# Optimization experiments

Measured on AMD Instinct MI355X. Metric: run time of the kernel, lower is better.

Reference implementation:

```python
import jax, jax.numpy as jnp
import numpy as np

HEADS = 8
DIM = 512
DIM_HEAD = 64          # dim // 8
LANDMARKS = 256        # dim // 2
PINV_ITERS = 6
KERNEL = 33            # residual_conv_kernel
SCALE = DIM_HEAD ** -0.5
LN_EPS = 1e-5


def _moore_penrose_pinv(x, iters):
    # x: [B,H,m,m]; global (over all batches/heads) max of row/col abs sums, as in torch impl
    abs_x = jnp.abs(x)
    col = abs_x.sum(-1).max()
    row = abs_x.sum(-2).max()
    z = jnp.swapaxes(x, -1, -2) / (col * row)
    I = jnp.eye(x.shape[-1], dtype=x.dtype)
    for _ in range(iters):
        xz = x @ z
        z = 0.25 * z @ (13.0 * I - (xz @ (15.0 * I - (xz @ (7.0 * I - xz)))))
    return z


def setup_inputs() -> dict:
    key = jax.random.key(0)
    ks = jax.random.split(key, 5)
    B, N = 4, 8192
    x = jax.random.normal(ks[0], (B, N, DIM), dtype=jnp.float32)
    ln_g = jnp.ones((DIM,), jnp.float32)
    ln_b = jnp.zeros((DIM,), jnp.float32)
    w_qkv = jax.random.normal(ks[1], (DIM, 3 * HEADS * DIM_HEAD), jnp.float32) * 0.02
    w_out = jax.random.normal(ks[2], (HEADS * DIM_HEAD, DIM), jnp.float32) * 0.02
    b_out = jnp.zeros((DIM,), jnp.float32)
    res_kernel = jax.random.normal(ks[3], (HEADS, 1, KERNEL, 1), jnp.float32) * 0.02  # OIHW depthwise
    return {"x": x, "ln_g": ln_g, "ln_b": ln_b, "w_qkv": w_qkv,
            "w_out": w_out, "b_out": b_out, "res_kernel": res_kernel}


def reference(x, ln_g, ln_b, w_qkv, w_out, b_out, res_kernel):
    B, N, D = x.shape
    # pre-norm LayerNorm
    mu = x.mean(-1, keepdims=True)
    var = jnp.mean((x - mu) ** 2, axis=-1, keepdims=True)
    xn = (x - mu) * jax.lax.rsqrt(var + LN_EPS) * ln_g + ln_b
    # left-pad sequence so it divides into LANDMARKS groups (torch pads at front)
    m = LANDMARKS
    pad = (m - N % m) % m
    xp = jnp.pad(xn, ((0, 0), (pad, 0), (0, 0)))
    Np = N + pad
    qkv = xp @ w_qkv                                    # [B,Np,3*H*dh]
    q, k, v = jnp.split(qkv, 3, axis=-1)
    split_heads = lambda t: t.reshape(B, Np, HEADS, DIM_HEAD).transpose(0, 2, 1, 3)
    q, k, v = split_heads(q), split_heads(k), split_heads(v)  # [B,H,Np,dh]
    q = q * SCALE
    l = Np // m                                         # landmark group size
    q_l = q.reshape(B, HEADS, m, l, DIM_HEAD).sum(3) / l  # [B,H,m,dh]
    k_l = k.reshape(B, HEADS, m, l, DIM_HEAD).sum(3) / l
    sim1 = jnp.einsum('bhid,bhjd->bhij', q, k_l)        # [B,H,Np,m]
    sim2 = jnp.einsum('bhid,bhjd->bhij', q_l, k_l)      # [B,H,m,m]
    sim3 = jnp.einsum('bhid,bhjd->bhij', q_l, k)        # [B,H,m,Np]
    attn1 = jax.nn.softmax(sim1, axis=-1)
    attn2 = jax.nn.softmax(sim2, axis=-1)
    attn3 = jax.nn.softmax(sim3, axis=-1)
    attn2_inv = _moore_penrose_pinv(attn2, PINV_ITERS)
    out = (attn1 @ attn2_inv) @ (attn3 @ v)             # [B,H,Np,dh]
    # depthwise conv residual over sequence dim (Conv2d kernel (33,1), groups=heads)
    res = jax.lax.conv_general_dilated(
        v, res_kernel, window_strides=(1, 1),
        padding=[(KERNEL // 2, KERNEL // 2), (0, 0)],
        dimension_numbers=('NCHW', 'OIHW', 'NCHW'),
        feature_group_count=HEADS)
    out = out + res
    out = out.transpose(0, 2, 1, 3).reshape(B, Np, HEADS * DIM_HEAD)
    out = out @ w_out + b_out                           # dropout = identity (eval)
    out = out[:, -N:]                                   # drop front padding
    return x + out
```

## Files before the change

### kernel.cpp

```cpp
#include <hip/hip_runtime.h>
#include <hip/hip_bf16.h>
#include <stdint.h>

#define B_ 4
#define H_ 8
#define N_ 8192
#define D_ 512
#define M_ 256
#define BH 32
#define TOK 32768
#define SCALE 0.125f
#define LN_EPS 1e-5f

using bf16x8 = __attribute__((ext_vector_type(8))) short;
using f32x4  = __attribute__((ext_vector_type(4))) float;
typedef unsigned short u16;
typedef unsigned int   u32;

__device__ __forceinline__ float bf2f(u16 h){ union{u32 u; float f;} x; x.u = ((u32)h)<<16; return x.f; }
__device__ __forceinline__ u16 f2bf(float f){ union{float f; u32 u;} x; x.f=f; u32 r = (x.u + 0x7fffu + ((x.u>>16)&1u))>>16; return (u16)r; }
__device__ __forceinline__ f32x4 mfma16(bf16x8 a, bf16x8 b, f32x4 c){
  return __builtin_amdgcn_mfma_f32_16x16x32_bf16(a, b, c, 0, 0, 0);
}
__device__ __forceinline__ void stage16(const u16* g, u16* lds){
  __builtin_amdgcn_global_load_lds((const __attribute__((address_space(1))) unsigned int*)g,
                                   (__attribute__((address_space(3))) unsigned int*)lds, 16, 0, 0);
}

__global__ __launch_bounds__(256) void k_prep(const float* __restrict__ wqkv, const float* __restrict__ wout,
                                              u16* __restrict__ wqkvt, u16* __restrict__ woutt){
  int id = blockIdx.x*256 + threadIdx.x;
  for (int i = id; i < 1536*512; i += gridDim.x*256){ int c = i>>9, kk = i&511; wqkvt[i] = f2bf(wqkv[(size_t)kk*1536 + c]); }
  for (int i = id; i < 512*512;  i += gridDim.x*256){ int c = i>>9, kk = i&511; woutt[i] = f2bf(wout[(size_t)kk*512 + c]); }
}

__global__ __launch_bounds__(256) void k_ln(const float* __restrict__ x, const float* __restrict__ g,
                                            const float* __restrict__ bb, u16* __restrict__ xn){
  int row = blockIdx.x; int tid = threadIdx.x;
  const float* xr = x + (size_t)row*D_;
  float2 v = reinterpret_cast<const float2*>(xr)[tid];
  float s1 = v.x + v.y, s2 = v.x*v.x + v.y*v.y;
  for (int o=1;o<64;o<<=1){ s1 += __shfl_xor(s1,o); s2 += __shfl_xor(s2,o); }
  __shared__ float a1[4], a2[4];
  if ((tid&63)==0){ a1[tid>>6]=s1; a2[tid>>6]=s2; }
  __syncthreads();
  s1 = a1[0]+a1[1]+a1[2]+a1[3]; s2 = a2[0]+a2[1]+a2[2]+a2[3];
  float mu = s1*(1.f/D_);
  float var = s2*(1.f/D_) - mu*mu;
  float rs = rsqrtf(var + LN_EPS);
  float2 gg = reinterpret_cast<const float2*>(g)[tid];
  float2 b2 = reinterpret_cast<const float2*>(bb)[tid];
  u16 o0 = f2bf((v.x-mu)*rs*gg.x + b2.x);
  u16 o1 = f2bf((v.y-mu)*rs*gg.y + b2.y);
  reinterpret_cast<u32*>(xn + (size_t)row*D_)[tid] = (u32)o0 | ((u32)o1<<16);
}

__global__ __launch_bounds__(256) void k_qkv(const u16* __restrict__ A, const u16* __restrict__ Bt,
    u16* __restrict__ q, u16* __restrict__ k, u16* __restrict__ vt){
  __shared__ __align__(16) u16 As[2][128*32];
  __shared__ __align__(16) u16 Bs[2][128*32];
  int m0 = blockIdx.x*128, n0 = blockIdx.y*128;
  int tid = threadIdx.x, lane = tid&63, wave = tid>>6;
  int wm = wave>>1, wn = wave&1;
  int lr = lane>>2, lc = (lane&3)*8;
  f32x4 acc[4][4];
  #pragma unroll
  for (int i=0;i<4;i++)
    #pragma unroll
    for (int j=0;j<4;j++) acc[i][j] = (f32x4)0.f;

  auto stage_tile = [&](int k0, int buf){
    #pragma unroll
    for (int i=0;i<2;i++){
      int c = wave + i*4;
      stage16(&A [(size_t)(m0 + c*16 + lr)*512 + k0 + lc], &As[buf][c*16*32]);
      stage16(&Bt[(size_t)(n0 + c*16 + lr)*512 + k0 + lc], &Bs[buf][c*16*32]);
    }
  };
  stage_tile(0, 0);
  for (int it=0; it<16; it++){
    int cur = it&1;
    if (it<15){
      stage_tile((it+1)*32, cur^1);
      asm volatile("s_waitcnt vmcnt(4)" ::: "memory");
    } else {
      asm volatile("s_waitcnt vmcnt(0)" ::: "memory");
    }
    __syncthreads();
    bf16x8 a[4], b[4];
    #pragma unroll
    for (int mi=0;mi<4;mi++) a[mi] = *reinterpret_cast<const bf16x8*>(&As[cur][(wm*64+mi*16+(lane&15))*32 + (lane>>4)*8]);
    #pragma unroll
    for (int ni=0;ni<4;ni++) b[ni] = *reinterpret_cast<const bf16x8*>(&Bs[cur][(wn*64+ni*16+(lane&15))*32 + (lane>>4)*8]);
    #pragma unroll
    for (int mi=0;mi<4;mi++)
      #pragma unroll
      for (int ni=0;ni<4;ni++)
        acc[mi][ni] = mfma16(a[mi], b[ni], acc[mi][ni]);
    __syncthreads();
  }
  #pragma unroll
  for (int mi=0;mi<4;mi++){
    int gr0 = m0 + wm*64 + mi*16 + ((lane>>4)<<2);
    #pragma unroll
    for (int ni=0;ni<4;ni++){
      int gc = n0 + wn*64 + ni*16 + (lane&15);
      int t = gc>>9, wi = gc&511, h = wi>>6, d = wi&63;
      #pragma unroll
      for (int r=0;r<4;r++){
        int row = gr0 + r; int bq = row>>13, n = row & (N_-1);
        float val = acc[mi][ni][r];
        size_t bhh = (size_t)(bq*H_+h);
        if (t==0)      q[(bhh*N_ + n)*64 + d] = f2bf(val*SCALE);
        else if (t==1) k[(bhh*N_ + n)*64 + d] = f2bf(val);
        else           vt[(bhh*64 + d)*N_ + n] = f2bf(val);
      }
    }
  }
}

__global__ __launch_bounds__(64) void k_land(const u16* __restrict__ q, const u16* __restrict__ k,
                                             u16* __restrict__ ql, u16* __restrict__ kl){
  int bh = blockIdx.x >> 8, j = blockIdx.x & 255, d = threadIdx.x;
  size_t base = ((size_t)bh*N_ + j*32)*64 + d;
  float sq=0.f, sk=0.f;
  #pragma unroll
  for (int i=0;i<32;i++){ sq += bf2f(q[base + (size_t)i*64]); sk += bf2f(k[base + (size_t)i*64]); }
  size_t o = ((size_t)bh*256 + j)*64 + d;
  ql[o] = f2bf(sq*(1.f/32.f)); kl[o] = f2bf(sk*(1.f/32.f));
}

__global__ __launch_bounds__(256) void k_attn2(const u16* __restrict__ ql, const u16* __restrict__ kl,
                                               float* __restrict__ X, float* __restrict__ Xt){
  int bh = blockIdx.x >> 8, i = blockIdx.x & 255, j = threadIdx.x;
  __shared__ float qrow[64];
  __shared__ float red[256];
  if (j < 64) qrow[j] = bf2f(ql[((size_t)bh*256+i)*64 + j]);
  __syncthreads();
  const u16* kr = kl + ((size_t)bh*256 + j)*64;
  float s = 0.f;
  #pragma unroll
  for (int d=0; d<64; d++) s += qrow[d]*bf2f(kr[d]);
  red[j] = s; __syncthreads();
  for (int o=128;o>0;o>>=1){ if (j<o) red[j] = fmaxf(red[j], red[j+o]); __syncthreads(); }
  float mx = red[0]; __syncthreads();
  float e = __expf(s - mx);
  red[j] = e; __syncthreads();
  for (int o=128;o>0;o>>=1){ if (j<o) red[j] += red[j+o]; __syncthreads(); }
  float p = e / red[0];
  X [((size_t)bh*256+i)*256 + j] = p;
  Xt[((size_t)bh*256+j)*256 + i] = p;
}

__global__ __launch_bounds__(256) void k_pinvstats(const float* __restrict__ X, float* __restrict__ sc){
  int bh = blockIdx.x, t = threadIdx.x;
  const float* Xb = X + ((size_t)bh<<16);
  float cs=0.f, rs=0.f;
  for (int i=0;i<256;i++) cs += Xb[(size_t)i*256 + t];
  for (int j=0;j<256;j++) rs += Xb[(size_t)t*256 + j];
  __shared__ float r1[256], r2[256];
  r1[t]=cs; r2[t]=rs; __syncthreads();
  for (int o=128;o>0;o>>=1){ if (t<o){ r1[t]=fmaxf(r1[t],r1[t+o]); r2[t]=fmaxf(r2[t],r2[t+o]); } __syncthreads(); }
  if (t==0) sc[bh] = 1.f/(r1[0]*r2[0]);
}

__global__ __launch_bounds__(256) void k_pinvinit(const float* __restrict__ X, const float* __restrict__ Xt,
     const float* __restrict__ sc, u16* Xhi, u16* Xlo, u16* Znhi, u16* Znlo, u16* Zthi, u16* Ztlo){
  size_t i = (size_t)blockIdx.x*256 + threadIdx.x;
  int bh = (int)(i>>16);
  float s = sc[bh];
  float xv = X[i];  u16 h1 = f2bf(xv);  Xhi[i]=h1;  Xlo[i]=f2bf(xv - bf2f(h1));
  float zn = Xt[i]*s; u16 h2 = f2bf(zn); Znhi[i]=h2; Znlo[i]=f2bf(zn - bf2f(h2));
  float zt = xv*s;  u16 h3 = f2bf(zt);  Zthi[i]=h3; Ztlo[i]=f2bf(zt - bf2f(h3));
}

template<int MODE>
__global__ __launch_bounds__(256) void k_mmhl(
    const u16* Ahi, const u16* Alo,
    const u16* Bthi, const u16* Btlo,
    u16* Chi, u16* Clo,
    const u16* Znhi, const u16* Znlo,
    const u16* B1hi, const u16* B1lo,
    const u16* B2hi, const u16* B2lo,
    u16* Zothi, u16* Zotlo)
{
  __shared__ __align__(16) u16 AhS[2][64*32];
  __shared__ __align__(16) u16 AlS[2][64*32];
  __shared__ __align__(16) u16 BhS[2][64*32];
  __shared__ __align__(16) u16 BlS[2][64*32];
  int bh = blockIdx.z;
  int m0 = blockIdx.x*64, n0 = blockIdx.y*64;
  size_t base = ((size_t)bh)<<16;
  int tid = threadIdx.x, lane = tid&63, wave = tid>>6;
  int wm = wave>>1, wn = wave&1;
  int lr = lane>>2, lc = (lane&3)*8;
  f32x4 acc[2][2];
  #pragma unroll
  for (int i=0;i<2;i++)
    #pragma unroll
    for (int j=0;j<2;j++) acc[i][j] = (f32x4)0.f;

  auto stage_tile = [&](int k0, int buf){
    stage16(&Ahi [base + (size_t)(m0 + wave*16 + lr)*256 + k0 + lc], &AhS[buf][wave*16*32]);
    stage16(&Alo [base + (size_t)(m0 + wave*16 + lr)*256 + k0 + lc], &AlS[buf][wave*16*32]);
    stage16(&Bthi[base + (size_t)(n0 + wave*16 + lr)*256 + k0 + lc], &BhS[buf][wave*16*32]);
    stage16(&Btlo[base + (size_t)(n0 + wave*16 + lr)*256 + k0 + lc], &BlS[buf][wave*16*32]);
  };
  stage_tile(0, 0);
  for (int it=0; it<8; it++){
    int cur = it&1;
    if (it<7){
      stage_tile((it+1)*32, cur^1);
      asm volatile("s_waitcnt vmcnt(4)" ::: "memory");
    } else {
      asm volatile("s_waitcnt vmcnt(0)" ::: "memory");
    }
    __syncthreads();
    bf16x8 ah[2], al2[2], bh2[2], bl2[2];
    #pragma unroll
    for (int mi=0;mi<2;mi++){
      int rr = wm*32 + mi*16 + (lane&15);
      ah[mi]  = *reinterpret_cast<const bf16x8*>(&AhS[cur][rr*32 + (lane>>4)*8]);
      al2[mi] = *reinterpret_cast<const bf16x8*>(&AlS[cur][rr*32 + (lane>>4)*8]);
    }
    #pragma unroll
    for (int ni=0;ni<2;ni++){
      int rr = wn*32 + ni*16 + (lane&15);
      bh2[ni] = *reinterpret_cast<const bf16x8*>(&BhS[cur][rr*32 + (lane>>4)*8]);
      bl2[ni] = *reinterpret_cast<const bf16x8*>(&BlS[cur][rr*32 + (lane>>4)*8]);
    }
    #pragma unroll
    for (int mi=0;mi<2;mi++)
      #pragma unroll
      for (int ni=0;ni<2;ni++){
        f32x4 c = acc[mi][ni];
        c = mfma16(ah[mi],  bh2[ni], c);
        c = mfma16(ah[mi],  bl2[ni], c);
        c = mfma16(al2[mi], bh2[ni], c);
        acc[mi][ni] = c;
      }
    __syncthreads();
  }
  #pragma unroll
  for (int mi=0;mi<2;mi++){
    #pragma unroll
    for (int ni=0;ni<2;ni++){
      int gr0 = m0 + wm*32 + mi*16 + ((lane>>4)<<2);
      int gc  = n0 + wn*32 + ni*16 + (lane&15);
      #pragma unroll
      for (int rr=0;rr<4;rr++){
        int gr = gr0 + rr;
        float val = acc[mi][ni][rr];
        if (MODE==0){
          size_t o = base + (size_t)gr*256 + gc;
          u16 hh = f2bf(val); Chi[o]=hh; Clo[o]=f2bf(val - bf2f(hh));
        } else if (MODE==1){
          size_t o = base + (size_t)gc*256 + gr;
          u16 hh = f2bf(val); Chi[o]=hh; Clo[o]=f2bf(val - bf2f(hh));
        } else {
          size_t o = base + (size_t)gr*256 + gc;
          float z  = bf2f(Znhi[o]) + bf2f(Znlo[o]);
          float b1 = bf2f(B1hi[o]) + bf2f(B1lo[o]);
          float b2 = bf2f(B2hi[o]) + bf2f(B2lo[o]);
          float zn = 0.25f*(13.f*z - 15.f*b1 + 7.f*b2 - val);
          u16 hh = f2bf(zn); u16 ll = f2bf(zn - bf2f(hh));
          Chi[o] = hh; Clo[o] = ll;
          size_t ot = base + (size_t)gc*256 + gr;
          Zothi[ot] = hh; Zotlo[ot] = ll;
        }
      }
    }
  }
}

__global__ __launch_bounds__(256) void k_flashw(const u16* __restrict__ ql, const u16* __restrict__ kb,
                                                const u16* __restrict__ vt,
                                                float* __restrict__ part, float* __restrict__ lpart){
  __shared__ __align__(16) u16 P[4][64][40];
  int kc = blockIdx.x, bh = blockIdx.y;
  int tid = threadIdx.x, lane = tid&63, wave = tid>>6;
  bf16x8 aq[4][2];
  #pragma unroll
  for (int mi=0;mi<4;mi++){
    int row = wave*64 + mi*16 + (lane&15);
    #pragma unroll
    for (int ks=0;ks<2;ks++)
      aq[mi][ks] = *reinterpret_cast<const bf16x8*>(&ql[((size_t)bh*256 + row)*64 + ks*32 + (lane>>4)*8]);
  }
  f32x4 acc[4][4];
  float rs[4][4];
  #pragma unroll
  for (int i=0;i<4;i++)
    #pragma unroll
    for (int j=0;j<4;j++){ acc[i][j] = (f32x4)0.f; rs[i][j] = 0.f; }
  for (int step=0; step<16; step++){
    int nb = kc*512 + step*32;
    f32x4 s[4][2];
    #pragma unroll
    for (int ci=0;ci<2;ci++){
      int j = nb + ci*16 + (lane&15);
      const u16* kr = &kb[((size_t)bh*N_ + j)*64 + (lane>>4)*8];
      bf16x8 b0 = *reinterpret_cast<const bf16x8*>(kr);
      bf16x8 b1 = *reinterpret_cast<const bf16x8*>(kr + 32);
      #pragma unroll
      for (int mi=0;mi<4;mi++)
        s[mi][ci] = mfma16(aq[mi][1], b1, mfma16(aq[mi][0], b0, (f32x4)0.f));
    }
    #pragma unroll
    for (int mi=0;mi<4;mi++)
      #pragma unroll
      for (int ci=0;ci<2;ci++)
        #pragma unroll
        for (int rr=0;rr<4;rr++){
          float e = __expf(s[mi][ci][rr]);
          rs[mi][rr] += e;
          P[wave][mi*16 + ((lane>>4)<<2) + rr][ci*16 + (lane&15)] = f2bf(e);
        }
    __syncthreads();
    bf16x8 ap[4];
    #pragma unroll
    for (int mi=0;mi<4;mi++)
      ap[mi] = *reinterpret_cast<const bf16x8*>(&P[wave][mi*16 + (lane&15)][(lane>>4)*8]);
    #pragma unroll
    for (int ci=0;ci<4;ci++){
      int d = ci*16 + (lane&15);
      bf16x8 bv = *reinterpret_cast<const bf16x8*>(&vt[((size_t)bh*64 + d)*N_ + nb + (lane>>4)*8]);
      #pragma unroll
      for (int mi=0;mi<4;mi++)
        acc[mi][ci] = mfma16(ap[mi], bv, acc[mi][ci]);
    }
    __syncthreads();
  }
  #pragma unroll
  for (int mi=0;mi<4;mi++)
    #pragma unroll
    for (int rr=0;rr<4;rr++){
      float v2 = rs[mi][rr];
      v2 += __shfl_xor(v2,1); v2 += __shfl_xor(v2,2); v2 += __shfl_xor(v2,4); v2 += __shfl_xor(v2,8);
      rs[mi][rr] = v2;
    }
  size_t pb = ((size_t)kc*32 + bh)*256;
  #pragma unroll
  for (int mi=0;mi<4;mi++){
    int r0 = wave*64 + mi*16 + ((lane>>4)<<2);
    #pragma unroll
    for (int ci=0;ci<4;ci++){
      int d = ci*16 + (lane&15);
      #pragma unroll
      for (int rr=0;rr<4;rr++)
        part[(pb + r0 + rr)*64 + d] = acc[mi][ci][rr];
    }
    if ((lane&15)==0){
      #pragma unroll
      for (int rr=0;rr<4;rr++)
        lpart[pb + r0 + rr] = rs[mi][rr];
    }
  }
}

__global__ __launch_bounds__(256) void k_wfin(const float* __restrict__ part, const float* __restrict__ lpart,
                                              float* __restrict__ w){
  int idx = blockIdx.x*256 + threadIdx.x;
  int bh = idx>>14, within = idx & 16383, r = within>>6;
  float s = 0.f, l = 0.f;
  #pragma unroll
  for (int c=0;c<16;c++){
    s += part [(size_t)(c*32+bh)*16384 + within];
    l += lpart[(size_t)(c*32+bh)*256 + r];
  }
  w[idx] = s / l;
}

__global__ __launch_bounds__(64) void k_w2(const u16* __restrict__ Zhi, const u16* __restrict__ Zlo,
                                           const float* __restrict__ w, u16* __restrict__ w2t){
  int bh = blockIdx.x>>8, j = blockIdx.x&255, d = threadIdx.x;
  size_t zb = ((size_t)bh<<16) + (size_t)j*256;
  float acc = 0.f;
  for (int i=0;i<256;i++){
    float zv = bf2f(Zhi[zb+i]) + bf2f(Zlo[zb+i]);
    acc += zv * w[((size_t)bh*256 + i)*64 + d];
  }
  w2t[((size_t)bh*64 + d)*256 + j] = f2bf(acc);
}

__global__ __launch_bounds__(256) void k_conv(const u16* __restrict__ vt, const float* __restrict__ kern,
                                              u16* __restrict__ res_t){
  int t = threadIdx.x;
  int d = blockIdx.y, bh = blockIdx.z;
  int n0 = blockIdx.x*2048 + t*8;
  const u16* src = vt + ((size_t)bh*64 + d)*N_;
  const float* kh = kern + (bh&7)*33;
  float xv[40];
  #pragma unroll
  for (int vv=0; vv<5; vv++){
    int nb = n0 - 16 + vv*8;
    if (nb >= 0 && nb + 8 <= N_) {
      bf16x8 raw = *reinterpret_cast<const bf16x8*>(src + nb);
      #pragma unroll
      for (int j=0;j<8;j++) xv[vv*8+j] = bf2f((u16)raw[j]);
    } else {
      #pragma unroll
      for (int j=0;j<8;j++){
        int n = nb + j;
        xv[vv*8+j] = (n>=0 && n<N_) ? bf2f(src[n]) : 0.f;
      }
    }
  }
  float c[33];
  #pragma unroll
  for (int kk2=0;kk2<33;kk2++) c[kk2] = kh[kk2];
  u16 outv[8];
  #pragma unroll
  for (int j=0;j<8;j++){
    float acc = 0.f;
    #pragma unroll
    for (int kk2=0;kk2<33;kk2++) acc += xv[j+kk2]*c[kk2];
    outv[j] = f2bf(acc);
  }
  *reinterpret_cast<bf16x8*>(res_t + ((size_t)bh*64 + d)*N_ + n0) = *reinterpret_cast<bf16x8*>(outv);
}

__global__ __launch_bounds__(256) void k_attn1(const u16* __restrict__ q, const u16* __restrict__ kl,
   const u16* __restrict__ w2t, const u16* __restrict__ res_t, u16* __restrict__ cc)
{
  __shared__ __align__(16) u16 P[4][32][136];
  int n0 = blockIdx.x*128, bh = blockIdx.y;
  int tid = threadIdx.x, lane = tid&63, wave = tid>>6;
  int bq = bh>>3, h = bh&7;
  bf16x8 a[2][2];
  #pragma unroll
  for (int mi=0;mi<2;mi++){
    int n = n0 + wave*32 + mi*16 + (lane&15);
    #pragma unroll
    for (int ks=0;ks<2;ks++)
      a[mi][ks] = *reinterpret_cast<const bf16x8*>(&q[((size_t)bh*N_ + n)*64 + ks*32 + (lane>>4)*8]);
  }
  float rowsum[2][4];
  #pragma unroll
  for (int mi=0;mi<2;mi++)
    #pragma unroll
    for (int rr=0;rr<4;rr++) rowsum[mi][rr]=0.f;
  f32x4 acco[2][4];
  #pragma unroll
  for (int mi=0;mi<2;mi++)
    #pragma unroll
    for (int ci=0;ci<4;ci++) acco[mi][ci] = (f32x4)0.f;

  #pragma unroll
  for (int half=0; half<2; half++){
    f32x4 accs[2][8];
    #pragma unroll
    for (int mi=0;mi<2;mi++)
      #pragma unroll
      for (int ci=0;ci<8;ci++) accs[mi][ci] = (f32x4)0.f;
    #pragma unroll
    for (int ci=0;ci<8;ci++){
      int j = (half*8+ci)*16 + (lane&15);
      bf16x8 b0 = *reinterpret_cast<const bf16x8*>(&kl[((size_t)bh*256 + j)*64 + (lane>>4)*8]);
      bf16x8 b1 = *reinterpret_cast<const bf16x8*>(&kl[((size_t)bh*256 + j)*64 + 32 + (lane>>4)*8]);
      #pragma unroll
      for (int mi=0;mi<2;mi++){
        f32x4 c = accs[mi][ci];
        c = mfma16(a[mi][0], b0, c);
        c = mfma16(a[mi][1], b1, c);
        accs[mi][ci] = c;
      }
    }
    #pragma unroll
    for (int mi=0;mi<2;mi++)
      #pragma unroll
      for (int ci=0;ci<8;ci++)
        #pragma unroll
        for (int rr=0;rr<4;rr++){
          float e = __expf(accs[mi][ci][rr]);
          rowsum[mi][rr] += e;
          P[wave][mi*16 + ((lane>>4)<<2) + rr][ci*16 + (lane&15)] = f2bf(e);
        }
    __syncthreads();
    #pragma unroll
    for (int ks=0;ks<4;ks++){
      bf16x8 a2[2];
      #pragma unroll
      for (int mi=0;mi<2;mi++)
        a2[mi] = *reinterpret_cast<const bf16x8*>(&P[wave][mi*16 + (lane&15)][ks*32 + (lane>>4)*8]);
      #pragma unroll
      for (int ci=0;ci<4;ci++){
        bf16x8 b2 = *reinterpret_cast<const bf16x8*>(&w2t[((size_t)bh*64 + ci*16 + (lane&15))*256 + half*128 + ks*32 + (lane>>4)*8]);
        #pragma unroll
        for (int mi=0;mi<2;mi++)
          acco[mi][ci] = mfma16(a2[mi], b2, acco[mi][ci]);
      }
    }
    __syncthreads();
  }
  #pragma unroll
  for (int mi=0;mi<2;mi++)
    #pragma unroll
    for (int rr=0;rr<4;rr++){
      float s = rowsum[mi][rr];
      s += __shfl_xor(s,1); s += __shfl_xor(s,2); s += __shfl_xor(s,4); s += __shfl_xor(s,8);
      rowsum[mi][rr] = s;
    }
  #pragma unroll
  for (int mi=0;mi<2;mi++){
    int nb = n0 + wave*32 + mi*16 + ((lane>>4)<<2);
    #pragma unroll
    for (int ci=0;ci<4;ci++){
      int d = ci*16 + (lane&15);
      #pragma unroll
      for (int rr=0;rr<4;rr++){
        int n = nb + rr;
        float val = acco[mi][ci][rr] / rowsum[mi][rr];
        val += bf2f(res_t[((size_t)bh*64 + d)*N_ + n]);
        cc[((size_t)bq*N_ + n)*512 + h*64 + d] = f2bf(val);
      }
    }
  }
}

__global__ __launch_bounds__(256) void k_out(const u16* __restrict__ A, const u16* __restrict__ Bt,
     const float* __restrict__ bo, const float* __restrict__ x, float* __restrict__ out){
  __shared__ __align__(16) u16 As[2][128*32];
  __shared__ __align__(16) u16 Bs[2][128*32];
  int m0 = blockIdx.x*128, n0 = blockIdx.y*128;
  int tid = threadIdx.x, lane = tid&63, wave = tid>>6;
  int wm = wave>>1, wn = wave&1;
  int lr = lane>>2, lc = (lane&3)*8;
  f32x4 acc[4][4];
  #pragma unroll
  for (int i=0;i<4;i++)
    #pragma unroll
    for (int j=0;j<4;j++) acc[i][j] = (f32x4)0.f;

  auto stage_tile = [&](int k0, int buf){
    #pragma unroll
    for (int i=0;i<2;i++){
      int c = wave + i*4;
      stage16(&A [(size_t)(m0 + c*16 + lr)*512 + k0 + lc], &As[buf][c*16*32]);
      stage16(&Bt[(size_t)(n0 + c*16 + lr)*512 + k0 + lc], &Bs[buf][c*16*32]);
    }
  };
  stage_tile(0, 0);
  for (int it=0; it<16; it++){
    int cur = it&1;
    if (it<15){
      stage_tile((it+1)*32, cur^1);
      asm volatile("s_waitcnt vmcnt(4)" ::: "memory");
    } else {
      asm volatile("s_waitcnt vmcnt(0)" ::: "memory");
    }
    __syncthreads();
    bf16x8 a[4], b[4];
    #pragma unroll
    for (int mi=0;mi<4;mi++) a[mi] = *reinterpret_cast<const bf16x8*>(&As[cur][(wm*64+mi*16+(lane&15))*32 + (lane>>4)*8]);
    #pragma unroll
    for (int ni=0;ni<4;ni++) b[ni] = *reinterpret_cast<const bf16x8*>(&Bs[cur][(wn*64+ni*16+(lane&15))*32 + (lane>>4)*8]);
    #pragma unroll
    for (int mi=0;mi<4;mi++)
      #pragma unroll
      for (int ni=0;ni<4;ni++)
        acc[mi][ni] = mfma16(a[mi], b[ni], acc[mi][ni]);
    __syncthreads();
  }
  #pragma unroll
  for (int mi=0;mi<4;mi++){
    int gr0 = m0 + wm*64 + mi*16 + ((lane>>4)<<2);
    #pragma unroll
    for (int ni=0;ni<4;ni++){
      int gc = n0 + wn*64 + ni*16 + (lane&15);
      float bv = bo[gc];
      #pragma unroll
      for (int r=0;r<4;r++){
        int row = gr0 + r;
        out[(size_t)row*512 + gc] = acc[mi][ni][r] + bv + x[(size_t)row*512 + gc];
      }
    }
  }
}

extern "C" void kernel_launch(void* const* d_in, const int* in_sizes, int n_in,
                              void* d_out, int out_size, void* d_ws, size_t ws_size,
                              hipStream_t stream) {
  (void)in_sizes; (void)n_in; (void)out_size;
  const float* x     = (const float*)d_in[0];
  const float* ln_g  = (const float*)d_in[1];
  const float* ln_b  = (const float*)d_in[2];
  const float* w_qkv = (const float*)d_in[3];
  const float* w_out = (const float*)d_in[4];
  const float* b_out = (const float*)d_in[5];
  const float* res_k = (const float*)d_in[6];
  float* out = (float*)d_out;

  char* ws = (char*)d_ws;
  size_t off = 0;
  auto alloc = [&](size_t n)->char*{ char* r = ws + off; off += (n + 255) & ~(size_t)255; return r; };

  u16* xn     = (u16*)alloc((size_t)TOK*512*2);
  u16* cc     = xn;
  u16* wqkvt  = (u16*)alloc(1536*512*2);
  u16* woutt  = (u16*)alloc(512*512*2);
  u16* qb     = (u16*)alloc((size_t)BH*N_*64*2);
  u16* kb     = (u16*)alloc((size_t)BH*N_*64*2);
  u16* vt     = (u16*)alloc((size_t)BH*N_*64*2);
  u16* ql     = (u16*)alloc((size_t)BH*256*64*2);
  u16* kl     = (u16*)alloc((size_t)BH*256*64*2);
  float* X    = (float*)alloc((size_t)BH*65536*4);
  float* Xt   = (float*)alloc((size_t)BH*65536*4);
  float* sc   = (float*)alloc(32*4);
  u16* Xhi    = (u16*)alloc((size_t)BH*65536*2);
  u16* Xlo    = (u16*)alloc((size_t)BH*65536*2);
  u16* Znh    = (u16*)alloc((size_t)BH*65536*2);
  u16* Znl    = (u16*)alloc((size_t)BH*65536*2);
  u16* Zth    = (u16*)alloc((size_t)BH*65536*2);
  u16* Ztl    = (u16*)alloc((size_t)BH*65536*2);
  u16* B2h    = (u16*)alloc((size_t)BH*65536*2);
  u16* B2l    = (u16*)alloc((size_t)BH*65536*2);
  u16* res_t  = (u16*)alloc((size_t)BH*64*N_*2);
  size_t need = off;
  if (ws_size < need) return;

  u16* A1th = (u16*)X;
  u16* A1tl = (u16*)X + (size_t)BH*65536;
  u16* B1h  = (u16*)Xt;
  u16* B1l  = (u16*)Xt + (size_t)BH*65536;

  char* ob = (char*)d_out;
  float* part  = (float*)(ob);
  float* lpart = (float*)(ob + 33554432);
  float* wbuf  = (float*)(ob + 34078720);
  u16*   w2t   = (u16*)  (ob + 36175872);

  k_prep<<<dim3(512),256,0,stream>>>(w_qkv, w_out, wqkvt, woutt);
  k_ln<<<dim3(TOK),256,0,stream>>>(x, ln_g, ln_b, xn);
  k_qkv<<<dim3(256,12),256,0,stream>>>(xn, wqkvt, qb, kb, vt);
  k_land<<<dim3(8192),64,0,stream>>>(qb, kb, ql, kl);
  k_attn2<<<dim3(8192),256,0,stream>>>(ql, kl, X, Xt);
  k_pinvstats<<<dim3(32),256,0,stream>>>(X, sc);
  k_pinvinit<<<dim3(8192),256,0,stream>>>(X, Xt, sc, Xhi, Xlo, Znh, Znl, Zth, Ztl);

  dim3 gmm(4,4,32);
  for (int it=0; it<6; it++){
    k_mmhl<1><<<gmm,256,0,stream>>>(Xhi,Xlo, Zth,Ztl, A1th,A1tl,
        nullptr,nullptr,nullptr,nullptr,nullptr,nullptr, nullptr,nullptr);
    k_mmhl<0><<<gmm,256,0,stream>>>(Znh,Znl, A1th,A1tl, B1h,B1l,
        nullptr,nullptr,nullptr,nullptr,nullptr,nullptr, nullptr,nullptr);
    k_mmhl<0><<<gmm,256,0,stream>>>(B1h,B1l, A1th,A1tl, B2h,B2l,
        nullptr,nullptr,nullptr,nullptr,nullptr,nullptr, nullptr,nullptr);
    k_mmhl<2><<<gmm,256,0,stream>>>(B2h,B2l, A1th,A1tl, Znh,Znl,
        Znh,Znl, B1h,B1l, B2h,B2l, Zth,Ztl);
  }

  k_flashw<<<dim3(16,32),256,0,stream>>>(ql, kb, vt, part, lpart);
  k_wfin<<<dim3(2048),256,0,stream>>>(part, lpart, wbuf);
  k_w2<<<dim3(8192),64,0,stream>>>(Znh, Znl, wbuf, w2t);
  k_conv<<<dim3(4,64,32),256,0,stream>>>(vt, res_k, res_t);
  k_attn1<<<dim3(64,32),256,0,stream>>>(qb, kl, w2t, res_t, cc);
  k_out<<<dim3(256,4),256,0,stream>>>(cc, woutt, b_out, x, out);
}
```

Before: 1.043 ms.

## Triple-buffer GEMM staging, swizzle LDS layout, vectorize V-transpose stores

```diff
diff --git a/kernel.cpp b/kernel.cpp
--- a/kernel.cpp
+++ b/kernel.cpp
@@ -26,6 +26,8 @@
   __builtin_amdgcn_global_load_lds((const __attribute__((address_space(1))) unsigned int*)g,
                                    (__attribute__((address_space(3))) unsigned int*)lds, 16, 0, 0);
 }
+__device__ __forceinline__ int swz_src(int lane){ return (((lane&3) - (lane>>3)) & 3) * 8; }
+__device__ __forceinline__ int swz_ld(int row, int q){ return row*32 + (((q + (row>>1)) & 3) * 8); }
 
 __global__ __launch_bounds__(256) void k_prep(const float* __restrict__ wqkv, const float* __restrict__ wout,
                                               u16* __restrict__ wqkvt, u16* __restrict__ woutt){
@@ -57,12 +59,12 @@
 
 __global__ __launch_bounds__(256) void k_qkv(const u16* __restrict__ A, const u16* __restrict__ Bt,
     u16* __restrict__ q, u16* __restrict__ k, u16* __restrict__ vt){
-  __shared__ __align__(16) u16 As[2][128*32];
-  __shared__ __align__(16) u16 Bs[2][128*32];
+  __shared__ __align__(16) u16 As[3][128*32];
+  __shared__ __align__(16) u16 Bs[3][128*32];
   int m0 = blockIdx.x*128, n0 = blockIdx.y*128;
   int tid = threadIdx.x, lane = tid&63, wave = tid>>6;
   int wm = wave>>1, wn = wave&1;
-  int lr = lane>>2, lc = (lane&3)*8;
+  int lr = lane>>2, lcs = swz_src(lane);
   f32x4 acc[4][4];
   #pragma unroll
   for (int i=0;i<4;i++)
@@ -73,15 +75,18 @@
     #pragma unroll
     for (int i=0;i<2;i++){
       int c = wave + i*4;
-      stage16(&A [(size_t)(m0 + c*16 + lr)*512 + k0 + lc], &As[buf][c*16*32]);
-      stage16(&Bt[(size_t)(n0 + c*16 + lr)*512 + k0 + lc], &Bs[buf][c*16*32]);
+      stage16(&A [(size_t)(m0 + c*16 + lr)*512 + k0 + lcs], &As[buf][c*16*32]);
+      stage16(&Bt[(size_t)(n0 + c*16 + lr)*512 + k0 + lcs], &Bs[buf][c*16*32]);
     }
   };
   stage_tile(0, 0);
+  stage_tile(32, 1);
   for (int it=0; it<16; it++){
-    int cur = it&1;
-    if (it<15){
-      stage_tile((it+1)*32, cur^1);
+    int cur = it%3;
+    if (it<14){
+      stage_tile((it+2)*32, (it+2)%3);
+      asm volatile("s_waitcnt vmcnt(8)" ::: "memory");
+    } else if (it==14){
       asm volatile("s_waitcnt vmcnt(4)" ::: "memory");
     } else {
       asm volatile("s_waitcnt vmcnt(0)" ::: "memory");
@@ -89,9 +94,9 @@
     __syncthreads();
     bf16x8 a[4], b[4];
     #pragma unroll
-    for (int mi=0;mi<4;mi++) a[mi] = *reinterpret_cast<const bf16x8*>(&As[cur][(wm*64+mi*16+(lane&15))*32 + (lane>>4)*8]);
-    #pragma unroll
-    for (int ni=0;ni<4;ni++) b[ni] = *reinterpret_cast<const bf16x8*>(&Bs[cur][(wn*64+ni*16+(lane&15))*32 + (lane>>4)*8]);
+    for (int mi=0;mi<4;mi++) a[mi] = *reinterpret_cast<const bf16x8*>(&As[cur][swz_ld(wm*64+mi*16+(lane&15), lane>>4)]);
+    #pragma unroll
+    for (int ni=0;ni<4;ni++) b[ni] = *reinterpret_cast<const bf16x8*>(&Bs[cur][swz_ld(wn*64+ni*16+(lane&15), lane>>4)]);
     #pragma unroll
     for (int mi=0;mi<4;mi++)
       #pragma unroll
@@ -106,14 +111,21 @@
     for (int ni=0;ni<4;ni++){
       int gc = n0 + wn*64 + ni*16 + (lane&15);
       int t = gc>>9, wi = gc&511, h = wi>>6, d = wi&63;
-      #pragma unroll
-      for (int r=0;r<4;r++){
-        int row = gr0 + r; int bq = row>>13, n = row & (N_-1);
-        float val = acc[mi][ni][r];
-        size_t bhh = (size_t)(bq*H_+h);
-        if (t==0)      q[(bhh*N_ + n)*64 + d] = f2bf(val*SCALE);
-        else if (t==1) k[(bhh*N_ + n)*64 + d] = f2bf(val);
-        else           vt[(bhh*64 + d)*N_ + n] = f2bf(val);
+      size_t bhh0 = (size_t)((gr0>>13)*H_ + h);
+      if (t==2){
+        u16 pk[4];
+        #pragma unroll
+        for (int r=0;r<4;r++) pk[r] = f2bf(acc[mi][ni][r]);
+        int n = gr0 & (N_-1);
+        *reinterpret_cast<uint2*>(&vt[(bhh0*64 + d)*N_ + n]) = *reinterpret_cast<const uint2*>(pk);
+      } else {
+        #pragma unroll
+        for (int r=0;r<4;r++){
+          int row = gr0 + r; int n = row & (N_-1);
+          float val = acc[mi][ni][r];
+          if (t==0)      q[(bhh0*N_ + n)*64 + d] = f2bf(val*SCALE);
+          else           k[(bhh0*N_ + n)*64 + d] = f2bf(val);
+        }
       }
     }
   }
@@ -184,16 +196,16 @@
     const u16* B2hi, const u16* B2lo,
     u16* Zothi, u16* Zotlo)
 {
-  __shared__ __align__(16) u16 AhS[2][64*32];
-  __shared__ __align__(16) u16 AlS[2][64*32];
-  __shared__ __align__(16) u16 BhS[2][64*32];
-  __shared__ __align__(16) u16 BlS[2][64*32];
+  __shared__ __align__(16) u16 AhS[3][64*32];
+  __shared__ __align__(16) u16 AlS[3][64*32];
+  __shared__ __align__(16) u16 BhS[3][64*32];
+  __shared__ __align__(16) u16 BlS[3][64*32];
   int bh = blockIdx.z;
   int m0 = blockIdx.x*64, n0 = blockIdx.y*64;
   size_t base = ((size_t)bh)<<16;
   int tid = threadIdx.x, lane = tid&63, wave = tid>>6;
   int wm = wave>>1, wn = wave&1;
-  int lr = lane>>2, lc = (lane&3)*8;
+  int lr = lane>>2, lcs = swz_src(lane);
   f32x4 acc[2][2];
   #pragma unroll
   for (int i=0;i<2;i++)
@@ -201,16 +213,19 @@
     for (int j=0;j<2;j++) acc[i][j] = (f32x4)0.f;
 
   auto stage_tile = [&](int k0, int buf){
-    stage16(&Ahi [base + (size_t)(m0 + wave*16 + lr)*256 + k0 + lc], &AhS[buf][wave*16*32]);
-    stage16(&Alo [base + (size_t)(m0 + wave*16 + lr)*256 + k0 + lc], &AlS[buf][wave*16*32]);
-    stage16(&Bthi[base + (size_t)(n0 + wave*16 + lr)*256 + k0 + lc], &BhS[buf][wave*16*32]);
-    stage16(&Btlo[base + (size_t)(n0 + wave*16 + lr)*256 + k0 + lc], &BlS[buf][wave*16*32]);
+    stage16(&Ahi [base + (size_t)(m0 + wave*16 + lr)*256 + k0 + lcs], &AhS[buf][wave*16*32]);
+    stage16(&Alo [base + (size_t)(m0 + wave*16 + lr)*256 + k0 + lcs], &AlS[buf][wave*16*32]);
+    stage16(&Bthi[base + (size_t)(n0 + wave*16 + lr)*256 + k0 + lcs], &BhS[buf][wave*16*32]);
+    stage16(&Btlo[base + (size_t)(n0 + wave*16 + lr)*256 + k0 + lcs], &BlS[buf][wave*16*32]);
   };
   stage_tile(0, 0);
+  stage_tile(32, 1);
   for (int it=0; it<8; it++){
-    int cur = it&1;
-    if (it<7){
-      stage_tile((it+1)*32, cur^1);
+    int cur = it%3;
+    if (it<6){
+      stage_tile((it+2)*32, (it+2)%3);
+      asm volatile("s_waitcnt vmcnt(8)" ::: "memory");
+    } else if (it==6){
       asm volatile("s_waitcnt vmcnt(4)" ::: "memory");
     } else {
       asm volatile("s_waitcnt vmcnt(0)" ::: "memory");
@@ -220,14 +235,14 @@
     #pragma unroll
     for (int mi=0;mi<2;mi++){
       int rr = wm*32 + mi*16 + (lane&15);
-      ah[mi]  = *reinterpret_cast<const bf16x8*>(&AhS[cur][rr*32 + (lane>>4)*8]);
-      al2[mi] = *reinterpret_cast<const bf16x8*>(&AlS[cur][rr*32 + (lane>>4)*8]);
+      ah[mi]  = *reinterpret_cast<const bf16x8*>(&AhS[cur][swz_ld(rr, lane>>4)]);
+      al2[mi] = *reinterpret_cast<const bf16x8*>(&AlS[cur][swz_ld(rr, lane>>4)]);
     }
     #pragma unroll
     for (int ni=0;ni<2;ni++){
       int rr = wn*32 + ni*16 + (lane&15);
-      bh2[ni] = *reinterpret_cast<const bf16x8*>(&BhS[cur][rr*32 + (lane>>4)*8]);
-      bl2[ni] = *reinterpret_cast<const bf16x8*>(&BlS[cur][rr*32 + (lane>>4)*8]);
+      bh2[ni] = *reinterpret_cast<const bf16x8*>(&BhS[cur][swz_ld(rr, lane>>4)]);
+      bl2[ni] = *reinterpret_cast<const bf16x8*>(&BlS[cur][swz_ld(rr, lane>>4)]);
     }
     #pragma unroll
     for (int mi=0;mi<2;mi++)
@@ -520,12 +535,12 @@
 
 __global__ __launch_bounds__(256) void k_out(const u16* __restrict__ A, const u16* __restrict__ Bt,
      const float* __restrict__ bo, const float* __restrict__ x, float* __restrict__ out){
-  __shared__ __align__(16) u16 As[2][128*32];
-  __shared__ __align__(16) u16 Bs[2][128*32];
+  __shared__ __align__(16) u16 As[3][128*32];
+  __shared__ __align__(16) u16 Bs[3][128*32];
   int m0 = blockIdx.x*128, n0 = blockIdx.y*128;
   int tid = threadIdx.x, lane = tid&63, wave = tid>>6;
   int wm = wave>>1, wn = wave&1;
-  int lr = lane>>2, lc = (lane&3)*8;
+  int lr = lane>>2, lcs = swz_src(lane);
   f32x4 acc[4][4];
   #pragma unroll
   for (int i=0;i<4;i++)
@@ -536,15 +551,18 @@
     #pragma unroll
     for (int i=0;i<2;i++){
       int c = wave + i*4;
-      stage16(&A [(size_t)(m0 + c*16 + lr)*512 + k0 + lc], &As[buf][c*16*32]);
-      stage16(&Bt[(size_t)(n0 + c*16 + lr)*512 + k0 + lc], &Bs[buf][c*16*32]);
+      stage16(&A [(size_t)(m0 + c*16 + lr)*512 + k0 + lcs], &As[buf][c*16*32]);
+      stage16(&Bt[(size_t)(n0 + c*16 + lr)*512 + k0 + lcs], &Bs[buf][c*16*32]);
     }
   };
   stage_tile(0, 0);
+  stage_tile(32, 1);
   for (int it=0; it<16; it++){
-    int cur = it&1;
-    if (it<15){
-      stage_tile((it+1)*32, cur^1);
+    int cur = it%3;
+    if (it<14){
+      stage_tile((it+2)*32, (it+2)%3);
+      asm volatile("s_waitcnt vmcnt(8)" ::: "memory");
+    } else if (it==14){
       asm volatile("s_waitcnt vmcnt(4)" ::: "memory");
     } else {
       asm volatile("s_waitcnt vmcnt(0)" ::: "memory");
@@ -552,9 +570,9 @@
     __syncthreads();
     bf16x8 a[4], b[4];
     #pragma unroll
-    for (int mi=0;mi<4;mi++) a[mi] = *reinterpret_cast<const bf16x8*>(&As[cur][(wm*64+mi*16+(lane&15))*32 + (lane>>4)*8]);
-    #pragma unroll
-    for (int ni=0;ni<4;ni++) b[ni] = *reinterpret_cast<const bf16x8*>(&Bs[cur][(wn*64+ni*16+(lane&15))*32 + (lane>>4)*8]);
+    for (int mi=0;mi<4;mi++) a[mi] = *reinterpret_cast<const bf16x8*>(&As[cur][swz_ld(wm*64+mi*16+(lane&15), lane>>4)]);
+    #pragma unroll
+    for (int ni=0;ni<4;ni++) b[ni] = *reinterpret_cast<const bf16x8*>(&Bs[cur][swz_ld(wn*64+ni*16+(lane&15), lane>>4)]);
     #pragma unroll
     for (int mi=0;mi<4;mi++)
       #pragma unroll
```

Result: faster. 997.1 us (-4.4%).
